# Kernel optimization log

Measured on AMD Instinct MI355X. Metric: run time of the kernel, lower is better.

## Reference

```python
import jax, jax.numpy as jnp
import numpy as np

N_NODES = 100000
N_EDGES = 1600000


def setup_inputs() -> dict:
    key = jax.random.key(0)
    k1, k2, k3, k4 = jax.random.split(key, 4)
    x = jax.random.normal(k1, (N_NODES, 128), dtype=jnp.float32)
    edge_index = jax.random.randint(k2, (2, N_EDGES), 0, N_NODES, dtype=jnp.int64)
    # Glorot-ish init for weights
    W1 = jax.random.normal(k3, (128, 128), dtype=jnp.float32) * (1.0 / np.sqrt(128))
    b1 = jnp.zeros((128,), dtype=jnp.float32)
    W2 = jax.random.normal(k4, (128, 64), dtype=jnp.float32) * (1.0 / np.sqrt(128))
    b2 = jnp.zeros((64,), dtype=jnp.float32)
    return {"x": x, "edge_index": edge_index, "W1": W1, "b1": b1, "W2": W2, "b2": b2}


def _gcn_conv(x, src, dst, W, b):
    """PyG GCNConv: h = W x; symmetric deg^-1/2 norm over edges (incl. self-loops); scatter-add; + bias."""
    n = x.shape[0]
    h = x @ W  # [N, out]
    ones = jnp.ones(src.shape[0], dtype=h.dtype)
    deg = jax.ops.segment_sum(ones, dst, num_segments=n)  # in-degree incl self-loops
    dinv = jax.lax.rsqrt(jnp.maximum(deg, 1e-12))
    norm = dinv[src] * dinv[dst]  # [E+N]
    msg = h[src] * norm[:, None]  # [E+N, out] gather
    out = jax.ops.segment_sum(msg, dst, num_segments=n)  # scatter-add
    return out + b


def reference(x, edge_index, W1, b1, W2, b2):
    n = x.shape[0]
    loop = jnp.arange(n, dtype=edge_index.dtype)
    src = jnp.concatenate([edge_index[0], loop])  # add self-loops
    dst = jnp.concatenate([edge_index[1], loop])
    h = jax.nn.relu(_gcn_conv(x, src, dst, W1, b1))
    # dropout is identity in eval mode
    return _gcn_conv(h, src, dst, W2, b2)
```

## Files before the change

### kernel.cpp

```cpp
#include <hip/hip_runtime.h>
#include <hip/hip_bf16.h>
#include <hip/hip_fp16.h>

#define THREADS 256
#define BSHIFT 9
#define BIN_CHUNK 4096
#define KP 136
#define SRCMASK 0x1ffff

typedef __attribute__((ext_vector_type(8))) short bf16x8;
typedef __attribute__((ext_vector_type(8))) unsigned short u16x8;
typedef __attribute__((ext_vector_type(4))) float f32x4;


__device__ inline unsigned short f2bf(float f) {
    unsigned int u = __float_as_uint(f);
    unsigned int r = (u + 0x7fffu + ((u >> 16) & 1u)) >> 16;
    return (unsigned short)r;
}

__device__ inline float2 bf2_to_f2(unsigned int u) {
    float2 r;
    r.x = __uint_as_float(u << 16);
    r.y = __uint_as_float(u & 0xffff0000u);
    return r;
}

__device__ inline void accum_row(float* acc, uint4 v) {
    float2 a = bf2_to_f2(v.x), b = bf2_to_f2(v.y), c = bf2_to_f2(v.z), d = bf2_to_f2(v.w);
    acc[0] += a.x; acc[1] += a.y; acc[2] += b.x; acc[3] += b.y;
    acc[4] += c.x; acc[5] += c.y; acc[6] += d.x; acc[7] += d.y;
}

__device__ inline void accum_row_scaled(float* acc, uint4 v, float s) {
    float2 a = bf2_to_f2(v.x), b = bf2_to_f2(v.y), c = bf2_to_f2(v.z), d = bf2_to_f2(v.w);
    acc[0] = fmaf(s, a.x, acc[0]); acc[1] = fmaf(s, a.y, acc[1]);
    acc[2] = fmaf(s, b.x, acc[2]); acc[3] = fmaf(s, b.y, acc[3]);
    acc[4] = fmaf(s, c.x, acc[4]); acc[5] = fmaf(s, c.y, acc[5]);
    acc[6] = fmaf(s, d.x, acc[6]); acc[7] = fmaf(s, d.y, acc[7]);
}

__device__ inline float ep_dinv(int ep) {
    return __half2float(__ushort_as_half((unsigned short)((unsigned int)ep >> 17)));
}

__device__ inline bf16x8 load_bfrag(const float* __restrict__ W, int ldn, int k0, int col) {
    bf16x8 b;
#pragma unroll
    for (int i = 0; i < 8; ++i) b[i] = (short)f2bf(W[(size_t)(k0 + i) * ldn + col]);
    return b;
}


__global__ __launch_bounds__(256) void k_bin_gemm1(const int* __restrict__ src,
                                                   const int* __restrict__ dst,
                                                   int* __restrict__ bcur,
                                                   unsigned int* __restrict__ binned,
                                                   int E, int NB, int cap,
                                                   const float* __restrict__ x,
                                                   const float* __restrict__ W1,
                                                   unsigned short* __restrict__ h,
                                                   int M, int nbin) {
    __shared__ __align__(16) short As[64 * KP];
    const int t = threadIdx.x;

    if ((int)blockIdx.x < nbin) {
        int* bcnt = (int*)As;
        int* bres = bcnt + 256;
        bcnt[t] = 0;
        __syncthreads();
        int base = blockIdx.x * BIN_CHUNK;
        int sv[16], dv[16];
#pragma unroll
        for (int i = 0; i < 4; ++i) {
            int e0 = base + (i * 256 + t) * 4;
            if (e0 + 3 < E) {
                int4 s4 = *(const int4*)(src + e0);
                int4 d4 = *(const int4*)(dst + e0);
                sv[4 * i + 0] = s4.x; sv[4 * i + 1] = s4.y;
                sv[4 * i + 2] = s4.z; sv[4 * i + 3] = s4.w;
                dv[4 * i + 0] = d4.x; dv[4 * i + 1] = d4.y;
                dv[4 * i + 2] = d4.z; dv[4 * i + 3] = d4.w;
            } else {
                for (int k = 0; k < 4; ++k) {
                    int e = e0 + k;
                    if (e < E) { sv[4 * i + k] = src[e]; dv[4 * i + k] = dst[e]; }
                    else dv[4 * i + k] = -1;
                }
            }
        }
#pragma unroll
        for (int i = 0; i < 16; ++i)
            if (dv[i] >= 0) atomicAdd(&bcnt[dv[i] >> BSHIFT], 1);
        __syncthreads();
        if (t < NB) {
            int old = bcnt[t] ? atomicAdd(&bcur[t], bcnt[t]) : 0;
            bres[t] = t * cap + old;
        }
        __syncthreads();
#pragma unroll
        for (int i = 0; i < 16; ++i) {
            if (dv[i] >= 0) {
                int b = dv[i] >> BSHIFT;
                int pos = atomicAdd(&bres[b], 1);
                if (pos < (b + 1) * cap)
                    binned[pos] = ((unsigned int)(dv[i] & 511) << 23) | (unsigned int)sv[i];
            }
        }
        return;
    }

    const int m0 = ((int)blockIdx.x - nbin) * 64;
    {
        int ar = t >> 5;
        int ac = (t & 31) * 4;
#pragma unroll
        for (int rb = 0; rb < 64; rb += 8) {
            int lrow = rb + ar;
            int row = m0 + lrow;
            ushort4 sv = make_ushort4(0, 0, 0, 0);
            if (row < M) {
                float4 v = *(const float4*)(x + (size_t)row * 128 + ac);
                sv.x = f2bf(v.x); sv.y = f2bf(v.y); sv.z = f2bf(v.z); sv.w = f2bf(v.w);
            }
            *(ushort4*)&As[lrow * KP + ac] = sv;
        }
    }
    __syncthreads();

    const int w = t >> 6;
    const int lane = t & 63;
    const int lm = lane & 15;
    const int qd = lane >> 4;
    const int n0w = w * 32;

    f32x4 acc[4][2];
#pragma unroll
    for (int mi = 0; mi < 4; ++mi)
#pragma unroll
        for (int ni = 0; ni < 2; ++ni) acc[mi][ni] = (f32x4){0.f, 0.f, 0.f, 0.f};

#pragma unroll
    for (int ks = 0; ks < 4; ++ks) {
        bf16x8 b0 = load_bfrag(W1, 128, ks * 32 + qd * 8, n0w + lm);
        bf16x8 b1 = load_bfrag(W1, 128, ks * 32 + qd * 8, n0w + 16 + lm);
#pragma unroll
        for (int mi = 0; mi < 4; ++mi) {
            bf16x8 a = *(const bf16x8*)&As[(mi * 16 + lm) * KP + ks * 32 + qd * 8];
            acc[mi][0] = __builtin_amdgcn_mfma_f32_16x16x32_bf16(a, b0, acc[mi][0], 0, 0, 0);
            acc[mi][1] = __builtin_amdgcn_mfma_f32_16x16x32_bf16(a, b1, acc[mi][1], 0, 0, 0);
        }
    }

#pragma unroll
    for (int mi = 0; mi < 4; ++mi) {
#pragma unroll
        for (int ni = 0; ni < 2; ++ni) {
            int col = n0w + ni * 16 + lm;
#pragma unroll
            for (int r = 0; r < 4; ++r) {
                int lrow = mi * 16 + qd * 4 + r;
                int row = m0 + lrow;
                if (row < M) h[(size_t)row * 128 + col] = f2bf(acc[mi][ni][r]);
            }
        }
    }
}

__global__ __launch_bounds__(256) void k_node_place(const unsigned int* __restrict__ binned,
                                                    const int* __restrict__ bcur, int cap,
                                                    int* __restrict__ rp,
                                                    int* __restrict__ deg,
                                                    float* __restrict__ dinv,
                                                    int* __restrict__ eperm, int N,
                                                    const float* __restrict__ W2,
                                                    unsigned short* __restrict__ W2t, int NB) {
    int b = blockIdx.x;
    int t = threadIdx.x;
    if (b == NB) {
        for (int i = t; i < 64 * 128; i += 256) {
            int nn = i >> 7;
            int kk = i & 127;
            W2t[i] = f2bf(W2[(size_t)kk * 64 + nn]);
        }
        return;
    }
    __shared__ int lc[512];
    __shared__ int s[256];
    int beg = b * cap;
    int end = beg + min(bcur[b], cap);
    int d0 = b << BSHIFT;
    lc[t] = 0;
    lc[t + 256] = 0;
    __syncthreads();
    for (int j = beg + t; j < end; j += 256) atomicAdd(&lc[binned[j] >> 23], 1);
    __syncthreads();
    int a = lc[2 * t], c = lc[2 * t + 1];
    int pair = a + c;
    s[t] = pair;
    __syncthreads();
    for (int off = 1; off < 256; off <<= 1) {
        int add = (t >= off) ? s[t - off] : 0;
        __syncthreads();
        s[t] += add;
        __syncthreads();
    }
    int excl = s[t] - pair;
    int st0 = beg + excl, st1 = st0 + a;
    int node0 = d0 + 2 * t;
    if (node0 < N) {
        rp[node0] = st0;
        deg[node0] = a;
        dinv[node0] = rsqrtf((float)a + 1.0f);
    }
    if (node0 + 1 < N) {
        rp[node0 + 1] = st1;
        deg[node0 + 1] = c;
        dinv[node0 + 1] = rsqrtf((float)c + 1.0f);
    }
    __syncthreads();
    lc[2 * t] = st0;
    lc[2 * t + 1] = st1;
    __syncthreads();
    for (int j = beg + t; j < end; j += 256) {
        unsigned int p = binned[j];
        int pos = atomicAdd(&lc[p >> 23], 1);
        eperm[pos] = (int)(p & 0x7fffffu);
    }
}

__global__ __launch_bounds__(256) void k_pack(const int* __restrict__ bcur, int cap,
                                              const float* __restrict__ dinv,
                                              int* __restrict__ eperm) {
    int bkt = blockIdx.x >> 2, q = blockIdx.x & 3;
    int len = min(bcur[bkt], cap);
    int qlen = (len + 3) >> 2;
    int s = q * qlen;
    int e = min(s + qlen, len);
    int beg = bkt * cap;
    for (int j = beg + s + threadIdx.x; j < beg + e; j += 256) {
        int p = eperm[j];
        float dv = dinv[p];
        unsigned int hb = (unsigned int)__half_as_ushort(__float2half(dv));
        eperm[j] = (int)((unsigned int)p | (hb << 17));
    }
}


__global__ __launch_bounds__(256) void k_gather_gemm2(const int* __restrict__ rp,
                                                      const int* __restrict__ deg,
                                                      const int* __restrict__ eperm,
                                                      const float* __restrict__ dinv,
                                                      const uint4* __restrict__ h4,
                                                      const float* __restrict__ b1,
                                                      const unsigned short* __restrict__ W2t,
                                                      unsigned short* __restrict__ h2,
                                                      int n) {
    __shared__ __align__(16) short As[16 * KP];

    const int t = threadIdx.x;
    const int lane = t & 63;
    const int l16 = lane & 15;
    const int gbase = lane & 48;
    const int m0 = blockIdx.x * 16;
    const int lrow = (t >> 6) * 4 + (lane >> 4);
    const int node = m0 + lrow;
    const bool valid = node < n;

    int beg = 0, end = 0;
    float dv_self = 0.f;
    if (valid) {
        beg = rp[node];
        end = beg + deg[node];
        dv_self = dinv[node];
    }

    float acc[8];
#pragma unroll
    for (int i = 0; i < 8; ++i) acc[i] = 0.f;
    if (valid) accum_row_scaled(acc, h4[(size_t)node * 16 + l16], dv_self);

    for (int j = beg; j < end; j += 16) {
        int cnt = end - j;
        if (cnt > 16) cnt = 16;
        int ep = eperm[j + (l16 < cnt ? l16 : cnt - 1)];
        int k = 0;
        for (; k + 4 <= cnt; k += 4) {
            int e0 = __shfl(ep, gbase + k);
            int e1 = __shfl(ep, gbase + k + 1);
            int e2 = __shfl(ep, gbase + k + 2);
            int e3 = __shfl(ep, gbase + k + 3);
            uint4 v0 = h4[(size_t)(e0 & SRCMASK) * 16 + l16];
            uint4 v1 = h4[(size_t)(e1 & SRCMASK) * 16 + l16];
            uint4 v2 = h4[(size_t)(e2 & SRCMASK) * 16 + l16];
            uint4 v3 = h4[(size_t)(e3 & SRCMASK) * 16 + l16];
            accum_row_scaled(acc, v0, ep_dinv(e0));
            accum_row_scaled(acc, v1, ep_dinv(e1));
            accum_row_scaled(acc, v2, ep_dinv(e2));
            accum_row_scaled(acc, v3, ep_dinv(e3));
        }
        for (; k < cnt; ++k) {
            int e0 = __shfl(ep, gbase + k);
            uint4 v0 = h4[(size_t)(e0 & SRCMASK) * 16 + l16];
            accum_row_scaled(acc, v0, ep_dinv(e0));
        }
    }

    {
        float4 bb0 = ((const float4*)b1)[l16 * 2];
        float4 bb1 = ((const float4*)b1)[l16 * 2 + 1];
        u16x8 s;
        s[0] = f2bf(fmaxf(fmaf(dv_self, acc[0], bb0.x), 0.f));
        s[1] = f2bf(fmaxf(fmaf(dv_self, acc[1], bb0.y), 0.f));
        s[2] = f2bf(fmaxf(fmaf(dv_self, acc[2], bb0.z), 0.f));
        s[3] = f2bf(fmaxf(fmaf(dv_self, acc[3], bb0.w), 0.f));
        s[4] = f2bf(fmaxf(fmaf(dv_self, acc[4], bb1.x), 0.f));
        s[5] = f2bf(fmaxf(fmaf(dv_self, acc[5], bb1.y), 0.f));
        s[6] = f2bf(fmaxf(fmaf(dv_self, acc[6], bb1.z), 0.f));
        s[7] = f2bf(fmaxf(fmaf(dv_self, acc[7], bb1.w), 0.f));
        *(u16x8*)&As[lrow * KP + l16 * 8] = s;
    }
    __syncthreads();

    const int w = t >> 6;
    const int lm = lane & 15;
    const int qd = lane >> 4;
    const int col = w * 16 + lm;

    f32x4 c4 = (f32x4){0.f, 0.f, 0.f, 0.f};
#pragma unroll
    for (int ks = 0; ks < 4; ++ks) {
        bf16x8 b = *(const bf16x8*)&W2t[(size_t)col * 128 + ks * 32 + qd * 8];
        bf16x8 a = *(const bf16x8*)&As[lm * KP + ks * 32 + qd * 8];
        c4 = __builtin_amdgcn_mfma_f32_16x16x32_bf16(a, b, c4, 0, 0, 0);
    }

#pragma unroll
    for (int r = 0; r < 4; ++r) {
        int row = m0 + qd * 4 + r;
        if (row < n) h2[(size_t)row * 64 + col] = f2bf(dinv[row] * c4[r]);
    }
}

__global__ __launch_bounds__(256) void k_gather64(const int* __restrict__ rp,
                                                  const int* __restrict__ deg,
                                                  const int* __restrict__ eperm,
                                                  const float* __restrict__ dinv,
                                                  const uint4* __restrict__ h4,
                                                  const float* __restrict__ bias,
                                                  float* __restrict__ out, int n) {
    const int t = threadIdx.x;
    const int lane = t & 63;
    const int l8 = lane & 7;
    const int gbase = lane & 56;
    const int node = blockIdx.x * 32 + (t >> 6) * 8 + (lane >> 3);
    const bool valid = node < n;

    int beg = 0, end = 0;
    if (valid) {
        beg = rp[node];
        end = beg + deg[node];
    }

    float acc[8];
#pragma unroll
    for (int i = 0; i < 8; ++i) acc[i] = 0.f;
    if (valid) accum_row(acc, h4[(size_t)node * 8 + l8]);

    int j = beg;
    for (; j + 16 <= end; j += 16) {
        int ep0 = eperm[j + l8] & SRCMASK;
        int ep1 = eperm[j + 8 + l8] & SRCMASK;
        int idx[16];
#pragma unroll
        for (int k = 0; k < 8; ++k) idx[k] = __shfl(ep0, gbase + k);
#pragma unroll
        for (int k = 0; k < 8; ++k) idx[8 + k] = __shfl(ep1, gbase + k);
        uint4 v[16];
#pragma unroll
        for (int k = 0; k < 16; ++k) v[k] = h4[(size_t)idx[k] * 8 + l8];
#pragma unroll
        for (int k = 0; k < 16; ++k) accum_row(acc, v[k]);
    }
    int cnt = end - j;
    if (cnt >= 8) {
        int ep = eperm[j + l8] & SRCMASK;
        int idx[8];
#pragma unroll
        for (int k = 0; k < 8; ++k) idx[k] = __shfl(ep, gbase + k);
        uint4 v[8];
#pragma unroll
        for (int k = 0; k < 8; ++k) v[k] = h4[(size_t)idx[k] * 8 + l8];
#pragma unroll
        for (int k = 0; k < 8; ++k) accum_row(acc, v[k]);
        j += 8;
        cnt -= 8;
    }
    if (cnt > 0) {
        int ep = eperm[j + (l8 < cnt ? l8 : cnt - 1)] & SRCMASK;
        int k = 0;
        for (; k + 4 <= cnt; k += 4) {
            int i0 = __shfl(ep, gbase + k);
            int i1 = __shfl(ep, gbase + k + 1);
            int i2 = __shfl(ep, gbase + k + 2);
            int i3 = __shfl(ep, gbase + k + 3);
            uint4 v0 = h4[(size_t)i0 * 8 + l8];
            uint4 v1 = h4[(size_t)i1 * 8 + l8];
            uint4 v2 = h4[(size_t)i2 * 8 + l8];
            uint4 v3 = h4[(size_t)i3 * 8 + l8];
            accum_row(acc, v0);
            accum_row(acc, v1);
            accum_row(acc, v2);
            accum_row(acc, v3);
        }
        for (; k < cnt; ++k) {
            int i0 = __shfl(ep, gbase + k);
            uint4 v0 = h4[(size_t)i0 * 8 + l8];
            accum_row(acc, v0);
        }
    }

    if (valid) {
        float dv = dinv[node];
        float4 b0 = ((const float4*)bias)[l8 * 2];
        float4 b1 = ((const float4*)bias)[l8 * 2 + 1];
        float4 o0, o1;
        o0.x = dv * acc[0] + b0.x; o0.y = dv * acc[1] + b0.y;
        o0.z = dv * acc[2] + b0.z; o0.w = dv * acc[3] + b0.w;
        o1.x = dv * acc[4] + b1.x; o1.y = dv * acc[5] + b1.y;
        o1.z = dv * acc[6] + b1.z; o1.w = dv * acc[7] + b1.w;
        float4* orow = (float4*)(out + (size_t)node * 64);
        orow[l8 * 2] = o0;
        orow[l8 * 2 + 1] = o1;
    }
}


extern "C" void kernel_launch(void* const* d_in, const int* in_sizes, int n_in,
                              void* d_out, int out_size, void* d_ws, size_t ws_size,
                              hipStream_t stream) {
    const float* x  = (const float*)d_in[0];
    const int*   ei = (const int*)d_in[1];
    const float* W1 = (const float*)d_in[2];
    const float* b1 = (const float*)d_in[3];
    const float* W2 = (const float*)d_in[4];
    const float* b2 = (const float*)d_in[5];
    float* out = (float*)d_out;

    const int N = in_sizes[0] / 128;
    const int E = in_sizes[1] / 2;
    const int* src = ei;
    const int* dst = ei + E;
    const int NB = (N + 511) >> BSHIFT;
    const int cap = (E + NB - 1) / NB + ((E / NB) >> 2) + 1024;

    char* ws = (char*)d_ws;
    size_t off = 0;
    auto carve = [&](size_t bytes) -> void* {
        void* p = ws + off;
        off = (off + bytes + 255) & ~(size_t)255;
        return p;
    };
    float* dinv = (float*)carve((size_t)N * 4);
    int*   rp   = (int*)carve((size_t)N * 4);
    int*   deg  = (int*)carve((size_t)N * 4);
    int*   bcur = (int*)carve(256 * 4);
    unsigned int* binned = (unsigned int*)carve((size_t)NB * cap * 4);
    int*   eperm = (int*)carve((size_t)NB * cap * 4);
    unsigned short* h   = (unsigned short*)carve((size_t)N * 128 * 2);
    unsigned short* h2  = (unsigned short*)carve((size_t)N * 64 * 2);
    unsigned short* W2t = (unsigned short*)carve(64 * 128 * 2);

    const int gMm = (N + 63) / 64;
    const int nbin = (E + BIN_CHUNK - 1) / BIN_CHUNK;

    hipMemsetAsync(bcur, 0, 256 * sizeof(int), stream);
    k_bin_gemm1<<<nbin + gMm, THREADS, 0, stream>>>(src, dst, bcur, binned, E, NB, cap,
                                                    x, W1, h, N, nbin);
    k_node_place<<<NB + 1, THREADS, 0, stream>>>(binned, bcur, cap, rp, deg, dinv, eperm, N,
                                                 W2, W2t, NB);
    k_pack<<<NB * 4, THREADS, 0, stream>>>(bcur, cap, dinv, eperm);

    k_gather_gemm2<<<(N + 15) / 16, THREADS, 0, stream>>>(rp, deg, eperm, dinv, (const uint4*)h,
                                                          b1, W2t, h2, N);

    k_gather64<<<(N + 31) / 32, THREADS, 0, stream>>>(rp, deg, eperm, dinv, (const uint4*)h2, b2, out, N);
}
```

Measured before the change: 263.9 us.

## Prescale h by dinv in node_place, drop k_pack, stage binned writes in LDS

Removes the k_pack kernel that packed an fp16 dinv into each eperm entry. Instead k_node_place multiplies each node's bf16 h row by its own dinv, so the layer-1 gather becomes a plain sum of rows without per-edge scaling. Separately, the binning pass now sorts edges locally in shared memory and writes each bucket contiguously, giving more coalesced global stores to binned. Costs are an extra read-modify-write pass over h, an added bf16 rounding step, and an extra scan in the binning kernel.

```diff
diff --git a/kernel.cpp b/kernel.cpp
--- a/kernel.cpp
+++ b/kernel.cpp
@@ -1,12 +1,10 @@
 #include <hip/hip_runtime.h>
 #include <hip/hip_bf16.h>
-#include <hip/hip_fp16.h>
 
 #define THREADS 256
 #define BSHIFT 9
 #define BIN_CHUNK 4096
 #define KP 136
-#define SRCMASK 0x1ffff
 
 typedef __attribute__((ext_vector_type(8))) short bf16x8;
 typedef __attribute__((ext_vector_type(8))) unsigned short u16x8;
@@ -17,6 +15,10 @@
     unsigned int u = __float_as_uint(f);
     unsigned int r = (u + 0x7fffu + ((u >> 16) & 1u)) >> 16;
     return (unsigned short)r;
+}
+
+__device__ inline unsigned int pack_bf2(float x, float y) {
+    return (unsigned int)f2bf(x) | ((unsigned int)f2bf(y) << 16);
 }
 
 __device__ inline float2 bf2_to_f2(unsigned int u) {
@@ -32,16 +34,9 @@
     acc[4] += c.x; acc[5] += c.y; acc[6] += d.x; acc[7] += d.y;
 }
 
-__device__ inline void accum_row_scaled(float* acc, uint4 v, float s) {
-    float2 a = bf2_to_f2(v.x), b = bf2_to_f2(v.y), c = bf2_to_f2(v.z), d = bf2_to_f2(v.w);
-    acc[0] = fmaf(s, a.x, acc[0]); acc[1] = fmaf(s, a.y, acc[1]);
-    acc[2] = fmaf(s, b.x, acc[2]); acc[3] = fmaf(s, b.y, acc[3]);
-    acc[4] = fmaf(s, c.x, acc[4]); acc[5] = fmaf(s, c.y, acc[5]);
-    acc[6] = fmaf(s, d.x, acc[6]); acc[7] = fmaf(s, d.y, acc[7]);
-}
-
-__device__ inline float ep_dinv(int ep) {
-    return __half2float(__ushort_as_half((unsigned short)((unsigned int)ep >> 17)));
+__device__ inline unsigned int scale_bf2(unsigned int u, float s) {
+    float2 f = bf2_to_f2(u);
+    return pack_bf2(s * f.x, s * f.y);
 }
 
 __device__ inline bf16x8 load_bfrag(const float* __restrict__ W, int ldn, int k0, int col) {
@@ -61,12 +56,15 @@
                                                    const float* __restrict__ W1,
                                                    unsigned short* __restrict__ h,
                                                    int M, int nbin) {
-    __shared__ __align__(16) short As[64 * KP];
+    __shared__ __align__(16) char smem[20608];
     const int t = threadIdx.x;
 
     if ((int)blockIdx.x < nbin) {
-        int* bcnt = (int*)As;
+        int* bcnt = (int*)smem;
         int* bres = bcnt + 256;
+        int* loc  = bres + 256;
+        int* lcur = loc + 256;
+        unsigned int* staged = (unsigned int*)(lcur + 256);
         bcnt[t] = 0;
         __syncthreads();
         int base = blockIdx.x * BIN_CHUNK;
@@ -97,19 +95,41 @@
             int old = bcnt[t] ? atomicAdd(&bcur[t], bcnt[t]) : 0;
             bres[t] = t * cap + old;
         }
+        loc[t] = bcnt[t];
+        __syncthreads();
+        for (int off = 1; off < 256; off <<= 1) {
+            int add = (t >= off) ? loc[t - off] : 0;
+            __syncthreads();
+            loc[t] += add;
+            __syncthreads();
+        }
+        lcur[t] = loc[t] - bcnt[t];
         __syncthreads();
 #pragma unroll
         for (int i = 0; i < 16; ++i) {
             if (dv[i] >= 0) {
                 int b = dv[i] >> BSHIFT;
-                int pos = atomicAdd(&bres[b], 1);
-                if (pos < (b + 1) * cap)
-                    binned[pos] = ((unsigned int)(dv[i] & 511) << 23) | (unsigned int)sv[i];
+                int p = atomicAdd(&lcur[b], 1);
+                staged[p] = ((unsigned int)(dv[i] & 511) << 23) | (unsigned int)sv[i];
             }
         }
+        __syncthreads();
+        int wv = t >> 6, ln = t & 63;
+        for (int b = wv; b < 256; b += 4) {
+            int cnt = bcnt[b];
+            if (!cnt) continue;
+            int lst = loc[b] - cnt;
+            int gst = bres[b];
+            int gend = (b + 1) * cap;
+            for (int k = ln; k < cnt; k += 64) {
+                int g = gst + k;
+                if (g < gend) binned[g] = staged[lst + k];
+            }
+        }
         return;
     }
 
+    short* As = (short*)smem;
     const int m0 = ((int)blockIdx.x - nbin) * 64;
     {
         int ar = t >> 5;
@@ -174,7 +194,8 @@
                                                     float* __restrict__ dinv,
                                                     int* __restrict__ eperm, int N,
                                                     const float* __restrict__ W2,
-                                                    unsigned short* __restrict__ W2t, int NB) {
+                                                    unsigned short* __restrict__ W2t, int NB,
+                                                    uint4* __restrict__ h4) {
     int b = blockIdx.x;
     int t = threadIdx.x;
     if (b == NB) {
@@ -187,6 +208,7 @@
     }
     __shared__ int lc[512];
     __shared__ int s[256];
+    __shared__ float dvl[512];
     int beg = b * cap;
     int end = beg + min(bcur[b], cap);
     int d0 = b << BSHIFT;
@@ -208,15 +230,19 @@
     int excl = s[t] - pair;
     int st0 = beg + excl, st1 = st0 + a;
     int node0 = d0 + 2 * t;
+    float dv0 = rsqrtf((float)a + 1.0f);
+    float dv1 = rsqrtf((float)c + 1.0f);
+    dvl[2 * t] = dv0;
+    dvl[2 * t + 1] = dv1;
     if (node0 < N) {
         rp[node0] = st0;
         deg[node0] = a;
-        dinv[node0] = rsqrtf((float)a + 1.0f);
+        dinv[node0] = dv0;
     }
     if (node0 + 1 < N) {
         rp[node0 + 1] = st1;
         deg[node0 + 1] = c;
-        dinv[node0 + 1] = rsqrtf((float)c + 1.0f);
+        dinv[node0 + 1] = dv1;
     }
     __syncthreads();
     lc[2 * t] = st0;
@@ -227,22 +253,19 @@
         int pos = atomicAdd(&lc[p >> 23], 1);
         eperm[pos] = (int)(p & 0x7fffffu);
     }
-}
-
-__global__ __launch_bounds__(256) void k_pack(const int* __restrict__ bcur, int cap,
-                                              const float* __restrict__ dinv,
-                                              int* __restrict__ eperm) {
-    int bkt = blockIdx.x >> 2, q = blockIdx.x & 3;
-    int len = min(bcur[bkt], cap);
-    int qlen = (len + 3) >> 2;
-    int s = q * qlen;
-    int e = min(s + qlen, len);
-    int beg = bkt * cap;
-    for (int j = beg + s + threadIdx.x; j < beg + e; j += 256) {
-        int p = eperm[j];
-        float dv = dinv[p];
-        unsigned int hb = (unsigned int)__half_as_ushort(__float2half(dv));
-        eperm[j] = (int)((unsigned int)p | (hb << 17));
+    int nrows = min(512, N - d0);
+    if (nrows > 0) {
+        for (int j = t; j < nrows * 16; j += 256) {
+            int r = j >> 4, cidx = j & 15;
+            size_t idx = (size_t)(d0 + r) * 16 + cidx;
+            uint4 v = h4[idx];
+            float sdv = dvl[r];
+            v.x = scale_bf2(v.x, sdv);
+            v.y = scale_bf2(v.y, sdv);
+            v.z = scale_bf2(v.z, sdv);
+            v.w = scale_bf2(v.w, sdv);
+            h4[idx] = v;
+        }
     }
 }
 
@@ -278,7 +301,7 @@
     float acc[8];
 #pragma unroll
     for (int i = 0; i < 8; ++i) acc[i] = 0.f;
-    if (valid) accum_row_scaled(acc, h4[(size_t)node * 16 + l16], dv_self);
+    if (valid) accum_row(acc, h4[(size_t)node * 16 + l16]);
 
     for (int j = beg; j < end; j += 16) {
         int cnt = end - j;
@@ -290,19 +313,19 @@
             int e1 = __shfl(ep, gbase + k + 1);
             int e2 = __shfl(ep, gbase + k + 2);
             int e3 = __shfl(ep, gbase + k + 3);
-            uint4 v0 = h4[(size_t)(e0 & SRCMASK) * 16 + l16];
-            uint4 v1 = h4[(size_t)(e1 & SRCMASK) * 16 + l16];
-            uint4 v2 = h4[(size_t)(e2 & SRCMASK) * 16 + l16];
-            uint4 v3 = h4[(size_t)(e3 & SRCMASK) * 16 + l16];
-            accum_row_scaled(acc, v0, ep_dinv(e0));
-            accum_row_scaled(acc, v1, ep_dinv(e1));
-            accum_row_scaled(acc, v2, ep_dinv(e2));
-            accum_row_scaled(acc, v3, ep_dinv(e3));
+            uint4 v0 = h4[(size_t)e0 * 16 + l16];
+            uint4 v1 = h4[(size_t)e1 * 16 + l16];
+            uint4 v2 = h4[(size_t)e2 * 16 + l16];
+            uint4 v3 = h4[(size_t)e3 * 16 + l16];
+            accum_row(acc, v0);
+            accum_row(acc, v1);
+            accum_row(acc, v2);
+            accum_row(acc, v3);
         }
         for (; k < cnt; ++k) {
             int e0 = __shfl(ep, gbase + k);
-            uint4 v0 = h4[(size_t)(e0 & SRCMASK) * 16 + l16];
-            accum_row_scaled(acc, v0, ep_dinv(e0));
+            uint4 v0 = h4[(size_t)e0 * 16 + l16];
+            accum_row(acc, v0);
         }
     }
 
@@ -369,8 +392,8 @@
 
     int j = beg;
     for (; j + 16 <= end; j += 16) {
-        int ep0 = eperm[j + l8] & SRCMASK;
-        int ep1 = eperm[j + 8 + l8] & SRCMASK;
+        int ep0 = eperm[j + l8];
+        int ep1 = eperm[j + 8 + l8];
         int idx[16];
 #pragma unroll
         for (int k = 0; k < 8; ++k) idx[k] = __shfl(ep0, gbase + k);
@@ -384,7 +407,7 @@
     }
     int cnt = end - j;
     if (cnt >= 8) {
-        int ep = eperm[j + l8] & SRCMASK;
+        int ep = eperm[j + l8];
         int idx[8];
 #pragma unroll
         for (int k = 0; k < 8; ++k) idx[k] = __shfl(ep, gbase + k);
@@ -397,7 +420,7 @@
         cnt -= 8;
     }
     if (cnt > 0) {
-        int ep = eperm[j + (l8 < cnt ? l8 : cnt - 1)] & SRCMASK;
+        int ep = eperm[j + (l8 < cnt ? l8 : cnt - 1)];
         int k = 0;
         for (; k + 4 <= cnt; k += 4) {
             int i0 = __shfl(ep, gbase + k);
@@ -478,8 +501,7 @@
     k_bin_gemm1<<<nbin + gMm, THREADS, 0, stream>>>(src, dst, bcur, binned, E, NB, cap,
                                                     x, W1, h, N, nbin);
     k_node_place<<<NB + 1, THREADS, 0, stream>>>(binned, bcur, cap, rp, deg, dinv, eperm, N,
-                                                 W2, W2t, NB);
-    k_pack<<<NB * 4, THREADS, 0, stream>>>(bcur, cap, dinv, eperm);
+                                                 W2, W2t, NB, (uint4*)h);
 
     k_gather_gemm2<<<(N + 15) / 16, THREADS, 0, stream>>>(rp, deg, eperm, dinv, (const uint4*)h,
                                                           b1, W2t, h2, N);
```

Result: no change. 264.9 us (+0.4%).
